# Kernel tuning notes

Hardware: AMD Instinct MI355X
Metric: run time of the kernel (lower is better)

Reference implementation:

```python
import jax, jax.numpy as jnp
import numpy as np

NUM_NODES = 500000
D = 128      # embedding_size
U = 32       # embedding_u_size
T = 4        # edge_type_count
A = 32       # dim_a
N_SRC = 65536
B = 8192
E = 262144   # edges per edge type
EPS = 1e-12  # F.normalize eps


def setup_inputs() -> dict:
    key = jax.random.key(0)
    ks = jax.random.split(key, 9)
    std = 1.0 / np.sqrt(D).astype(np.float32)
    node_embeddings = jax.random.uniform(ks[0], (NUM_NODES, D), minval=-1.0, maxval=1.0, dtype=jnp.float32)
    node_type_embeddings = jax.random.uniform(ks[1], (NUM_NODES, T, U), minval=-1.0, maxval=1.0, dtype=jnp.float32)
    trans_w = jax.random.normal(ks[2], (T, U, D), dtype=jnp.float32) * std
    trans_w_s1 = jax.random.normal(ks[3], (T, U, A), dtype=jnp.float32) * std
    trans_w_s2 = jax.random.normal(ks[4], (T, A, 1), dtype=jnp.float32) * std
    input_nodes = jax.random.randint(ks[5], (N_SRC,), 0, NUM_NODES, dtype=jnp.int32)
    output_nodes = jax.random.randint(ks[6], (B,), 0, NUM_NODES, dtype=jnp.int32)
    edge_src = jax.random.randint(ks[7], (T, E), 0, N_SRC, dtype=jnp.int32)
    edge_dst = jax.random.randint(ks[8], (T, E), 0, B, dtype=jnp.int32)
    return {
        "node_embeddings": node_embeddings,
        "node_type_embeddings": node_type_embeddings,
        "trans_w": trans_w,
        "trans_w_s1": trans_w_s1,
        "trans_w_s2": trans_w_s2,
        "input_nodes": input_nodes,
        "output_nodes": output_nodes,
        "edge_src": edge_src,
        "edge_dst": edge_dst,
    }


def reference(node_embeddings, node_type_embeddings, trans_w, trans_w_s1,
              trans_w_s2, input_nodes, output_nodes, edge_src, edge_dst):
    # Gather per-type embeddings of the src frontier: [N_src, T, U]
    feats = node_type_embeddings[input_nodes]
    # Per-edge-type messages: for type t, feats[edge_src[t], t] -> [T, E, U]
    msgs = feats[edge_src, jnp.arange(T)[:, None]]
    # Sum aggregation into dst nodes (copy_u / sum): [T, B, U]
    agg = jax.vmap(lambda m, d: jax.ops.segment_sum(m, d, num_segments=B))(msgs, edge_dst)
    nte = agg.transpose(1, 0, 2)  # [B, T, U] node_type_embed

    # tanh-attention over edge types
    h = jnp.tanh(jnp.einsum('btu,tua->bta', nte, trans_w_s1))    # [B, T, A]
    scores = jnp.einsum('bta,ta->bt', h, trans_w_s2[..., 0])     # [B, T]
    att = jax.nn.softmax(scores, axis=1)                         # [B, T]
    combined = jnp.einsum('bt,btu->bu', att, nte)                # [B, U]

    # Per-type transform of the shared combined vector: [B, T, D]
    trans = jnp.einsum('bu,tud->btd', combined, trans_w)
    out = node_embeddings[output_nodes][:, None, :] + trans      # [B, T, D]
    norm = jnp.linalg.norm(out, axis=2, keepdims=True)
    return out / jnp.maximum(norm, EPS)
```

## Files before the change

kernel.cpp:

```cpp
#include <hip/hip_runtime.h>
#include <hip/hip_bf16.h>

#define NUM_NODES 500000
#define DD  128
#define UU  32
#define TT  4
#define AA  32
#define NSRC 65536
#define BB  8192
#define EE  262144
#define NEDGE (TT * EE)
#define NBKT (BB * TT)
#define CAP 128
#define AGG_FLOATS (BB * TT * UU)
#define NB  16

__device__ __forceinline__ unsigned short f2bf(float f) {
    unsigned int u = __float_as_uint(f);
    unsigned int r = (u + 0x7FFFu + ((u >> 16) & 1u)) >> 16;
    return (unsigned short)r;
}

__global__ __launch_bounds__(256) void prep_kernel(
    const float4* __restrict__ nte4,
    const int* __restrict__ input_nodes,
    unsigned short* __restrict__ feats,
    int* __restrict__ cnt,
    int* __restrict__ ovfCnt)
{
    int b = blockIdx.x;
    if (b < 32) {
        int i = b * 256 + threadIdx.x;
        ((int4*)cnt)[i] = make_int4(0, 0, 0, 0);
        if (b == 0 && threadIdx.x == 0) *ovfCnt = 0;
        return;
    }
    int gtid = (b - 32) * 256 + threadIdx.x;
    int src = gtid >> 5;
    int t = (gtid >> 3) & 3;
    int q = gtid & 7;
    long node = input_nodes[src];
    float4 v = nte4[node * 32 + t * 8 + q];
    ushort4 o;
    o.x = f2bf(v.x); o.y = f2bf(v.y); o.z = f2bf(v.z); o.w = f2bf(v.w);
    *(ushort4*)(feats + (((size_t)t * NSRC + src) << 5) + (q << 2)) = o;
}

__global__ __launch_bounds__(256) void place_kernel(
    const int* __restrict__ edge_src,
    const int* __restrict__ edge_dst,
    int* __restrict__ cnt,
    int* __restrict__ slots,
    int* __restrict__ ovfCnt,
    int* __restrict__ ovf)
{
    int i = blockIdx.x * 256 + threadIdx.x;
    int k = edge_dst[i] * 4 + (i >> 18);
    int src = edge_src[i];
    int pos = atomicAdd(&cnt[k], 1);
    if (pos < CAP) {
        slots[k * CAP + pos] = src;
    } else {
        int o = atomicAdd(ovfCnt, 1);
        ovf[2 * o] = k; ovf[2 * o + 1] = src;
    }
}

__global__ __launch_bounds__(1024) void gather_node_kernel(
    const unsigned short* __restrict__ feats,
    const int* __restrict__ slots,
    const int* __restrict__ cnt,
    const int* __restrict__ ovf,
    const int* __restrict__ ovfCnt,
    const float* __restrict__ node_emb,
    const float* __restrict__ w,
    const float* __restrict__ s1,
    const float* __restrict__ s2,
    const int* __restrict__ output_nodes,
    float* __restrict__ out)
{
    __shared__ float s_nte[NB][TT * UU];
    __shared__ float s_comb[NB][UU];
    __shared__ float s_sc[NB][TT];
    __shared__ int   s_node[NB];
    __shared__ int   s_ovf;

    int tid  = threadIdx.x;
    int wv   = tid >> 6;
    int lane = tid & 63;
    int b0   = blockIdx.x * NB;
    int e8 = lane >> 3, q = lane & 7;

    {
        int dst = b0 + wv;
        #pragma unroll
        for (int t = 0; t < 4; ++t) {
            int k = dst * 4 + t;
            int n = cnt[k];
            int nslot = min(n, CAP);
            int pre = min(nslot, 64);
            int idx = slots[k * CAP + lane];
            const uint2* rows = (const uint2*)(feats + ((size_t)t * NSRC << 5)) + q;
            float a0 = 0.f, a1 = 0.f, a2 = 0.f, a3 = 0.f;
            int nIter = (pre + 7) >> 3;
            for (int it = 0; it < nIter; ++it) {
                int j = (it << 3) + e8;
                int s = __shfl(idx, j, 64);
                if (j < pre) {
                    uint2 vv = rows[(size_t)s * 8];
                    a0 += __uint_as_float(vv.x << 16);
                    a1 += __uint_as_float(vv.x & 0xffff0000u);
                    a2 += __uint_as_float(vv.y << 16);
                    a3 += __uint_as_float(vv.y & 0xffff0000u);
                }
            }
            for (int j = 64 + e8; j < nslot; j += 8) {
                int s = slots[k * CAP + j];
                uint2 vv = rows[(size_t)s * 8];
                a0 += __uint_as_float(vv.x << 16);
                a1 += __uint_as_float(vv.x & 0xffff0000u);
                a2 += __uint_as_float(vv.y << 16);
                a3 += __uint_as_float(vv.y & 0xffff0000u);
            }
            #pragma unroll
            for (int m = 8; m < 64; m <<= 1) {
                a0 += __shfl_xor(a0, m, 64);
                a1 += __shfl_xor(a1, m, 64);
                a2 += __shfl_xor(a2, m, 64);
                a3 += __shfl_xor(a3, m, 64);
            }
            if (lane < 8)
                ((float4*)&s_nte[wv][t * 32])[lane] = make_float4(a0, a1, a2, a3);
        }
    }
    if (tid < NB) s_node[tid] = output_nodes[b0 + tid];
    if (tid == 0) s_ovf = *ovfCnt;
    __syncthreads();

    if (s_ovf > 0) {
        for (int r = tid; r < s_ovf; r += 1024) {
            int k = ovf[2 * r];
            int dst = k >> 2;
            if (dst >= b0 && dst < b0 + NB) {
                int src = ovf[2 * r + 1];
                int t = k & 3, bl = dst - b0;
                const unsigned short* row = feats + (((size_t)t * NSRC + src) << 5);
                for (int u = 0; u < UU; ++u)
                    atomicAdd(&s_nte[bl][t * 32 + u],
                              __uint_as_float((unsigned)row[u] << 16));
            }
        }
        __syncthreads();
    }

    int a  = lane & 31;
    int th = lane >> 5;
    int t0 = th, t1 = th + 2;
    {
        int bl = wv;
        float acc0 = 0.f, acc1 = 0.f;
        #pragma unroll
        for (int u = 0; u < UU; ++u) {
            acc0 += s_nte[bl][t0 * UU + u] * s1[(t0 * UU + u) * AA + a];
            acc1 += s_nte[bl][t1 * UU + u] * s1[(t1 * UU + u) * AA + a];
        }
        float p0 = tanhf(acc0) * s2[t0 * AA + a];
        float p1 = tanhf(acc1) * s2[t1 * AA + a];
        #pragma unroll
        for (int m = 1; m < 32; m <<= 1) {
            p0 += __shfl_xor(p0, m, 64);
            p1 += __shfl_xor(p1, m, 64);
        }
        if ((lane & 31) == 0) { s_sc[bl][th] = p0; s_sc[bl][th + 2] = p1; }
    }
    __syncthreads();

    {
        int bl = wv;
        float sc0 = s_sc[bl][0], sc1 = s_sc[bl][1];
        float sc2 = s_sc[bl][2], sc3 = s_sc[bl][3];
        float mx = fmaxf(fmaxf(sc0, sc1), fmaxf(sc2, sc3));
        float e0 = expf(sc0 - mx), e1 = expf(sc1 - mx);
        float e2 = expf(sc2 - mx), e3 = expf(sc3 - mx);
        float isum = 1.f / (e0 + e1 + e2 + e3);
        if (lane < 32) {
            float c = e0 * isum * s_nte[bl][a]
                    + e1 * isum * s_nte[bl][UU + a]
                    + e2 * isum * s_nte[bl][2 * UU + a]
                    + e3 * isum * s_nte[bl][3 * UU + a];
            s_comb[bl][a] = c;
        }
    }
    __syncthreads();

    int t   = wv & 3;
    int grp = wv >> 2;
    const float* wt = w + t * (UU * DD);
    float wA[UU], wB[UU];
    #pragma unroll
    for (int u = 0; u < UU; ++u) {
        wA[u] = wt[u * DD + lane];
        wB[u] = wt[u * DD + lane + 64];
    }
    #pragma unroll
    for (int j = 0; j < 4; ++j) {
        int bl = grp * 4 + j;
        int node = s_node[bl];
        float accA = node_emb[(long)node * DD + lane];
        float accB = node_emb[(long)node * DD + lane + 64];
        #pragma unroll
        for (int u = 0; u < UU; ++u) {
            float c = s_comb[bl][u];
            accA += c * wA[u];
            accB += c * wB[u];
        }
        float sq = accA * accA + accB * accB;
        #pragma unroll
        for (int m = 1; m < 64; m <<= 1)
            sq += __shfl_xor(sq, m, 64);
        float invn = 1.f / fmaxf(sqrtf(sq), 1e-12f);
        int ob = (b0 + bl) * (TT * DD) + t * DD;
        out[ob + lane]      = accA * invn;
        out[ob + lane + 64] = accB * invn;
    }
}

__global__ __launch_bounds__(256) void zero_agg_kernel(float4* __restrict__ p) {
    int i = blockIdx.x * 256 + threadIdx.x;
    p[i] = make_float4(0.f, 0.f, 0.f, 0.f);
}

__global__ __launch_bounds__(256) void edge_atomic_kernel(
    const float* __restrict__ nte_in,
    const int* __restrict__ input_nodes,
    const int* __restrict__ edge_src,
    const int* __restrict__ edge_dst,
    float* __restrict__ agg)
{
    int tid = blockIdx.x * 256 + threadIdx.x;
    int i = tid >> 5;
    int u = tid & 31;
    int t = i >> 18;
    int src = edge_src[i];
    int dst = edge_dst[i];
    int node = input_nodes[src];
    float v = nte_in[(long)node * 128 + t * 32 + u];
    atomicAdd(&agg[dst * 128 + t * 32 + u], v);
}

__global__ __launch_bounds__(256) void node_kernel(
    const float* __restrict__ node_emb,
    const float* __restrict__ w,
    const float* __restrict__ s1,
    const float* __restrict__ s2,
    const int* __restrict__ output_nodes,
    const float* __restrict__ agg,
    float* __restrict__ out)
{
    __shared__ float s_nte[NB][TT * UU];
    __shared__ float s_comb[NB][UU];
    __shared__ float s_sc[NB][TT];
    __shared__ int   s_node[NB];

    int tid  = threadIdx.x;
    int wv   = tid >> 6;
    int lane = tid & 63;
    int b0   = blockIdx.x * NB;

    {
        const float4* av = (const float4*)(agg + b0 * 128);
        float4* sv = (float4*)&s_nte[0][0];
        sv[tid]       = av[tid];
        sv[tid + 256] = av[tid + 256];
    }
    if (tid < NB) s_node[tid] = output_nodes[b0 + tid];
    __syncthreads();

    int a  = lane & 31;
    int th = lane >> 5;
    int t0 = th, t1 = th + 2;
    float s1a[UU], s1b[UU];
    #pragma unroll
    for (int u = 0; u < UU; ++u) {
        s1a[u] = s1[(t0 * UU + u) * AA + a];
        s1b[u] = s1[(t1 * UU + u) * AA + a];
    }
    float s2a = s2[t0 * AA + a];
    float s2b = s2[t1 * AA + a];

    #pragma unroll
    for (int q = 0; q < 4; ++q) {
        int bl = wv * 4 + q;
        float acc0 = 0.f, acc1 = 0.f;
        #pragma unroll
        for (int u = 0; u < UU; ++u) {
            acc0 += s_nte[bl][t0 * UU + u] * s1a[u];
            acc1 += s_nte[bl][t1 * UU + u] * s1b[u];
        }
        float p0 = tanhf(acc0) * s2a;
        float p1 = tanhf(acc1) * s2b;
        #pragma unroll
        for (int m = 1; m < 32; m <<= 1) {
            p0 += __shfl_xor(p0, m, 64);
            p1 += __shfl_xor(p1, m, 64);
        }
        if ((lane & 31) == 0) { s_sc[bl][th] = p0; s_sc[bl][th + 2] = p1; }
    }
    __syncthreads();

    #pragma unroll
    for (int q = 0; q < 4; ++q) {
        int bl = wv * 4 + q;
        float sc0 = s_sc[bl][0], sc1 = s_sc[bl][1];
        float sc2 = s_sc[bl][2], sc3 = s_sc[bl][3];
        float mx = fmaxf(fmaxf(sc0, sc1), fmaxf(sc2, sc3));
        float e0 = expf(sc0 - mx), e1 = expf(sc1 - mx);
        float e2 = expf(sc2 - mx), e3 = expf(sc3 - mx);
        float isum = 1.f / (e0 + e1 + e2 + e3);
        if (lane < 32) {
            float c = e0 * isum * s_nte[bl][a]
                    + e1 * isum * s_nte[bl][UU + a]
                    + e2 * isum * s_nte[bl][2 * UU + a]
                    + e3 * isum * s_nte[bl][3 * UU + a];
            s_comb[bl][a] = c;
        }
    }
    __syncthreads();

    int t = wv;
    const float* wt = w + t * (UU * DD);
    float wA[UU], wB[UU];
    #pragma unroll
    for (int u = 0; u < UU; ++u) {
        wA[u] = wt[u * DD + lane];
        wB[u] = wt[u * DD + lane + 64];
    }
    for (int bl = 0; bl < NB; ++bl) {
        int node = s_node[bl];
        float accA = node_emb[(long)node * DD + lane];
        float accB = node_emb[(long)node * DD + lane + 64];
        #pragma unroll
        for (int u = 0; u < UU; ++u) {
            float c = s_comb[bl][u];
            accA += c * wA[u];
            accB += c * wB[u];
        }
        float sq = accA * accA + accB * accB;
        #pragma unroll
        for (int m = 1; m < 64; m <<= 1)
            sq += __shfl_xor(sq, m, 64);
        float invn = 1.f / fmaxf(sqrtf(sq), 1e-12f);
        int ob = (b0 + bl) * (TT * DD) + t * DD;
        out[ob + lane]      = accA * invn;
        out[ob + lane + 64] = accB * invn;
    }
}

extern "C" void kernel_launch(void* const* d_in, const int* in_sizes, int n_in,
                              void* d_out, int out_size, void* d_ws, size_t ws_size,
                              hipStream_t stream) {
    const float* node_emb = (const float*)d_in[0];
    const float* nte_in   = (const float*)d_in[1];
    const float* w        = (const float*)d_in[2];
    const float* s1       = (const float*)d_in[3];
    const float* s2       = (const float*)d_in[4];
    const int* input_nodes  = (const int*)d_in[5];
    const int* output_nodes = (const int*)d_in[6];
    const int* edge_src     = (const int*)d_in[7];
    const int* edge_dst     = (const int*)d_in[8];
    float* out = (float*)d_out;

    char* ws = (char*)d_ws;
    unsigned short* feats = (unsigned short*)ws;
    size_t off = (size_t)TT * NSRC * 32 * 2;
    int* slots  = (int*)(ws + off);          off += (size_t)NBKT * CAP * 4;
    int* cnt    = (int*)(ws + off);          off += (size_t)NBKT * 4;
    int* ovfCnt = (int*)(ws + off);          off += 256;
    int* ovf    = (int*)(ws + off);          off += (size_t)NEDGE * 2 * 4;
    size_t need = off;

    if (ws_size >= need) {
        prep_kernel<<<dim3(32 + TT * NSRC * 8 / 256), dim3(256), 0, stream>>>(
            (const float4*)nte_in, input_nodes, feats, cnt, ovfCnt);
        place_kernel<<<dim3(NEDGE / 256), dim3(256), 0, stream>>>(
            edge_src, edge_dst, cnt, slots, ovfCnt, ovf);
        gather_node_kernel<<<dim3(BB / NB), dim3(1024), 0, stream>>>(
            feats, slots, cnt, ovf, ovfCnt,
            node_emb, w, s1, s2, output_nodes, out);
    } else {
        float* agg = (float*)d_ws;
        zero_agg_kernel<<<dim3(AGG_FLOATS / 4 / 256), dim3(256), 0, stream>>>((float4*)agg);
        edge_atomic_kernel<<<dim3((NEDGE * 32) / 256), dim3(256), 0, stream>>>(
            nte_in, input_nodes, edge_src, edge_dst, agg);
        node_kernel<<<dim3(BB / NB), dim3(256), 0, stream>>>(
            node_emb, w, s1, s2, output_nodes, agg, out);
    }
}
```

Measured before the change: 114.7 us.

## Stage transform weights in LDS, shrink bucket capacity, and simplify slot gather

Copies the full trans_w tensor (64KB) into shared memory at block start and reads it from LDS in the output stage, replacing the 64 per-thread weight registers. This lowers register pressure so a higher occupancy hint can be used. CAP is halved to 64, which halves the slot buffer and sends more edges to the overflow path. The gather loop now loads each slot index directly instead of broadcasting it with a shuffle. The 64KB LDS per block may itself limit how many blocks fit per CU, and the launch-bounds hint of 8 may force register spills.

```diff
diff --git a/kernel.cpp b/kernel.cpp
--- a/kernel.cpp
+++ b/kernel.cpp
@@ -11,7 +11,7 @@
 #define EE  262144
 #define NEDGE (TT * EE)
 #define NBKT (BB * TT)
-#define CAP 128
+#define CAP 64
 #define AGG_FLOATS (BB * TT * UU)
 #define NB  16
 
@@ -66,7 +66,7 @@
     }
 }
 
-__global__ __launch_bounds__(1024) void gather_node_kernel(
+__global__ __launch_bounds__(1024, 8) void gather_node_kernel(
     const unsigned short* __restrict__ feats,
     const int* __restrict__ slots,
     const int* __restrict__ cnt,
@@ -79,6 +79,7 @@
     const int* __restrict__ output_nodes,
     float* __restrict__ out)
 {
+    __shared__ float s_w[TT][UU][DD];
     __shared__ float s_nte[NB][TT * UU];
     __shared__ float s_comb[NB][UU];
     __shared__ float s_sc[NB][TT];
@@ -92,35 +93,33 @@
     int e8 = lane >> 3, q = lane & 7;
 
     {
+        const float4* w4 = (const float4*)w;
+        float4* sw4 = (float4*)s_w;
+        #pragma unroll
+        for (int i = 0; i < 4; ++i)
+            sw4[tid + i * 1024] = w4[tid + i * 1024];
+    }
+
+    {
         int dst = b0 + wv;
         #pragma unroll
         for (int t = 0; t < 4; ++t) {
             int k = dst * 4 + t;
             int n = cnt[k];
             int nslot = min(n, CAP);
-            int pre = min(nslot, 64);
-            int idx = slots[k * CAP + lane];
             const uint2* rows = (const uint2*)(feats + ((size_t)t * NSRC << 5)) + q;
             float a0 = 0.f, a1 = 0.f, a2 = 0.f, a3 = 0.f;
-            int nIter = (pre + 7) >> 3;
+            int nIter = (nslot + 7) >> 3;
             for (int it = 0; it < nIter; ++it) {
                 int j = (it << 3) + e8;
-                int s = __shfl(idx, j, 64);
-                if (j < pre) {
+                if (j < nslot) {
+                    int s = slots[k * CAP + j];
                     uint2 vv = rows[(size_t)s * 8];
                     a0 += __uint_as_float(vv.x << 16);
                     a1 += __uint_as_float(vv.x & 0xffff0000u);
                     a2 += __uint_as_float(vv.y << 16);
                     a3 += __uint_as_float(vv.y & 0xffff0000u);
                 }
-            }
-            for (int j = 64 + e8; j < nslot; j += 8) {
-                int s = slots[k * CAP + j];
-                uint2 vv = rows[(size_t)s * 8];
-                a0 += __uint_as_float(vv.x << 16);
-                a1 += __uint_as_float(vv.x & 0xffff0000u);
-                a2 += __uint_as_float(vv.y << 16);
-                a3 += __uint_as_float(vv.y & 0xffff0000u);
             }
             #pragma unroll
             for (int m = 8; m < 64; m <<= 1) {
@@ -195,13 +194,6 @@
 
     int t   = wv & 3;
     int grp = wv >> 2;
-    const float* wt = w + t * (UU * DD);
-    float wA[UU], wB[UU];
-    #pragma unroll
-    for (int u = 0; u < UU; ++u) {
-        wA[u] = wt[u * DD + lane];
-        wB[u] = wt[u * DD + lane + 64];
-    }
     #pragma unroll
     for (int j = 0; j < 4; ++j) {
         int bl = grp * 4 + j;
@@ -211,8 +203,8 @@
         #pragma unroll
         for (int u = 0; u < UU; ++u) {
             float c = s_comb[bl][u];
-            accA += c * wA[u];
-            accB += c * wB[u];
+            accA += c * s_w[t][u][lane];
+            accB += c * s_w[t][u][lane + 64];
         }
         float sq = accA * accA + accB * accB;
         #pragma unroll
```

Measured after the change: 122.7 us. 7.0% more time.
